# Kernel tuning notes

Measured on AMD Instinct MI355X. Metric: run time of the kernel, lower is better.

Reference implementation:

```python
import jax, jax.numpy as jnp
import numpy as np

H = 2048      # hidden
QL = 768      # q lora rank
KVL = 512     # kv lora rank
DR = 64       # rope dim
DN = 128      # nope head dim
NH = 16       # attention heads
NIH = 8       # indexer heads
IDX = 128     # indexer key dim
BS = 16       # batch
BLK = 128     # cache block size
BPS = 32      # blocks per sequence
NB = BS * BPS # total cache blocks
MAXKV = BPS * BLK  # 4096 kv slots per seq
TOPK = 1024   # sparse attention budget


def rmsnorm(v, g, eps=1e-6):
    return v * jax.lax.rsqrt(jnp.mean(v * v, -1, keepdims=True) + eps) * g


def layernorm(v, g, b, eps=1e-6):
    c = v - jnp.mean(v, -1, keepdims=True)
    return c * jax.lax.rsqrt(jnp.mean(c * c, -1, keepdims=True) + eps) * g + b


def rope(v, sin, cos):
    h = v.shape[-1] // 2
    rot = jnp.concatenate([-v[..., h:], v[..., :h]], -1)
    return v * cos + rot * sin


def setup_inputs() -> dict:
    key = jax.random.key(0)
    ks = jax.random.split(key, 16)
    s = 0.02  # weight init scale
    ang = jax.random.uniform(ks[5], (BS, 1, DR)) * 6.2831853
    return dict(
        x=jax.random.normal(ks[0], (BS, 1, H)),
        w_dq=jax.random.normal(ks[1], (H, QL)) * s,
        w_uq_qr=jax.random.normal(ks[2], (QL, NH * (DN + DR))) * s,
        w_uk=jax.random.normal(ks[3], (NH, DN, KVL)) * s,
        w_dkv_kr=jax.random.normal(ks[4], (H, KVL + DR)) * s,
        gamma_cq=jnp.ones((QL,)),
        gamma_ckv=jnp.ones((KVL,)),
        sin=jnp.sin(ang),
        cos=jnp.cos(ang),
        cache_index=jnp.arange(BS, dtype=jnp.int32) * MAXKV,
        kv_cache=jax.random.normal(ks[6], (NB, BLK, KVL)),
        kr_cache=jax.random.normal(ks[7], (NB, BLK, DR)),
        block_table=jnp.arange(BS * BPS, dtype=jnp.int32).reshape(BS, BPS),
        act_seqs=jnp.full((BS,), MAXKV, dtype=jnp.int32),
        w_idx_qb=jax.random.normal(ks[8], (QL, NIH * IDX)) * s,
        w_idx_k=jax.random.normal(ks[9], (H, IDX)) * s,
        w_idx_proj=jax.random.normal(ks[10], (QL, NIH)) * s,
        in_gamma_k=jnp.ones((IDX,)),
        in_beta_k=jnp.zeros((IDX,)),
        index_k_cache=jax.random.normal(ks[11], (NB, BLK, IDX)),
    )


def reference(x, w_dq, w_uq_qr, w_uk, w_dkv_kr, gamma_cq, gamma_ckv, sin, cos,
              cache_index, kv_cache, kr_cache, block_table, act_seqs,
              w_idx_qb, w_idx_k, w_idx_proj, in_gamma_k, in_beta_k, index_k_cache):
    bs = x.shape[0]
    xq = x[:, 0]                      # [bs, H] (decode, q_len=1)
    s0, c0 = sin[:, 0], cos[:, 0]     # [bs, DR]

    # --- low-rank Q path ---
    cq = rmsnorm(xq @ w_dq, gamma_cq)                           # [bs, QL]
    q = (cq @ w_uq_qr).reshape(bs, NH, DN + DR)
    q_nope, q_pe = q[..., :DN], q[..., DN:]
    q_pe = rope(q_pe, s0[:, None, :], c0[:, None, :])           # [bs, NH, DR]

    # --- latent KV path + cache write ---
    ckv_kr = xq @ w_dkv_kr
    ckv = rmsnorm(ckv_kr[:, :KVL], gamma_ckv)                   # [bs, KVL]
    kr = rope(ckv_kr[:, KVL:], s0, c0)                          # [bs, DR]
    kv_flat = kv_cache.reshape(NB * BLK, KVL).at[cache_index].set(ckv)
    kr_flat = kr_cache.reshape(NB * BLK, DR).at[cache_index].set(kr)

    # --- lightning indexer ---
    ki = layernorm(xq @ w_idx_k, in_gamma_k, in_beta_k)         # [bs, IDX]
    ik_flat = index_k_cache.reshape(NB * BLK, IDX).at[cache_index].set(ki)
    qi = (cq @ w_idx_qb).reshape(bs, NIH, IDX)
    head_w = cq @ w_idx_proj                                    # [bs, NIH]

    # paged gather: flat slot ids per sequence position
    pos = (block_table * BLK)[:, :, None] + jnp.arange(BLK, dtype=block_table.dtype)
    pos = pos.reshape(bs, MAXKV)                                # [bs, MAXKV]
    ki_all = ik_flat[pos]                                       # [bs, MAXKV, IDX]

    isc = jax.nn.relu(jnp.einsum('bhd,bnd->bhn', qi, ki_all))
    isc = jnp.einsum('bh,bhn->bn', head_w, isc) / jnp.sqrt(jnp.float32(IDX))
    mask = jnp.arange(MAXKV)[None, :] < act_seqs[:, None]
    isc = jnp.where(mask, isc, -1e9)
    top_s, top_i = jax.lax.top_k(isc, TOPK)                     # [bs, TOPK]

    sel = jnp.take_along_axis(pos, top_i, axis=1)               # [bs, TOPK]
    ckv_sel = kv_flat[sel]                                      # [bs, TOPK, KVL]
    kr_sel = kr_flat[sel]                                       # [bs, TOPK, DR]

    # --- absorbed MLA attention over selected tokens ---
    q_lat = jnp.einsum('bhd,hdc->bhc', q_nope, w_uk)            # [bs, NH, KVL]
    scale = 1.0 / np.sqrt(DN + DR)
    att = (jnp.einsum('bhc,bnc->bhn', q_lat, ckv_sel)
           + jnp.einsum('bhr,bnr->bhn', q_pe, kr_sel)) * scale
    att = jnp.where((top_s > -1e8)[:, None, :], att, -1e9)
    p = jax.nn.softmax(att, axis=-1)                            # [bs, NH, TOPK]
    o_lat = jnp.einsum('bhn,bnc->bhc', p, ckv_sel)              # [bs, NH, KVL]
    o = jnp.einsum('bhc,hdc->bhd', o_lat, w_uk)                 # [bs, NH, DN]
    return o.reshape(bs, 1, NH * DN)
```

## Files before the change

kernel.cpp:

```cpp
#include <hip/hip_runtime.h>

typedef unsigned int u32;

#define BS    16
#define HDIM  2048
#define QL    768
#define KVL   512
#define DR    64
#define DN    128
#define NH    16
#define NIH   8
#define IDXD  128
#define BLK   128
#define BPS   32
#define MAXKV 4096
#define TOPK  1024
#define NCH   32

__global__ void k_dproj(const float* __restrict__ x, const float* __restrict__ w_dq,
                        const float* __restrict__ w_dkv, const float* __restrict__ w_ik,
                        float* __restrict__ dpart){
  int tile = blockIdx.x, ks = blockIdx.y, t = threadIdx.x;
  __shared__ float xs[16*128];
  __shared__ float sred[8*32*17];
  int k0 = ks*128;
  for (int idx=t; idx<16*128; idx+=256){
    int bb=idx>>7, kk=idx&127;
    xs[idx] = x[bb*HDIM + k0 + kk];
  }
  const float* wp; int ld, c0, gbase;
  if (tile < 24){ wp=w_dq;  ld=768; c0=tile*32;      gbase=0; }
  else if (tile < 42){ wp=w_dkv; ld=576; c0=(tile-24)*32; gbase=768; }
  else { wp=w_ik;  ld=128; c0=(tile-42)*32; gbase=1344; }
  int cl = t&31, kg = t>>5;
  int col = c0 + cl;
  __syncthreads();
  float acc[16];
  #pragma unroll
  for (int bb=0;bb<16;bb++) acc[bb]=0.f;
  const float* wb = wp + (size_t)(k0 + kg*16)*ld + col;
  #pragma unroll 4
  for (int kk=0; kk<16; kk++){
    float wv = wb[(size_t)kk*ld];
    int kx = kg*16+kk;
    #pragma unroll
    for (int bb=0; bb<16; bb++) acc[bb] += xs[bb*128+kx]*wv;
  }
  #pragma unroll
  for (int bb=0;bb<16;bb++) sred[(kg*32+cl)*17+bb] = acc[bb];
  __syncthreads();
  for (int r=0; r<2; r++){
    int o = r*256 + t;
    int bb = o>>5, cl2 = o&31;
    float s=0.f;
    #pragma unroll
    for (int kg2=0; kg2<8; kg2++) s += sred[(kg2*32+cl2)*17+bb];
    dpart[((size_t)ks*16 + bb)*1472 + gbase + c0 + cl2] = s;
  }
}

__global__ void k_dfin(const float* __restrict__ dpart, const float* __restrict__ g_cq,
                       const float* __restrict__ g_ckv, const float* __restrict__ sinp,
                       const float* __restrict__ cosp, const float* __restrict__ g_ik,
                       const float* __restrict__ b_ik, const int* __restrict__ cidx,
                       float* __restrict__ cq, float* __restrict__ kvc,
                       float* __restrict__ krc, float* __restrict__ ikc){
  int b = blockIdx.x, t = threadIdx.x;
  __shared__ float val[1472];
  __shared__ float red[256];
  for (int c=t; c<1472; c+=256){
    float s = 0.f;
    for (int ks2=0; ks2<16; ks2++) s += dpart[((size_t)ks2*16+b)*1472 + c];
    val[c] = s;
  }
  __syncthreads();
  float c0v = val[t], c1v = val[t+256], c2v = val[t+512];
  red[t] = c0v*c0v + c1v*c1v + c2v*c2v;
  __syncthreads();
  for (int s=128;s>0;s>>=1){ if(t<s) red[t]+=red[t+s]; __syncthreads(); }
  float scq = 1.0f/sqrtf(red[0]/(float)QL + 1e-6f);
  __syncthreads();
  float v0 = val[768+t], v1 = val[1024+t];
  red[t] = v0*v0 + v1*v1;
  __syncthreads();
  for (int s=128;s>0;s>>=1){ if(t<s) red[t]+=red[t+s]; __syncthreads(); }
  float sckv = 1.0f/sqrtf(red[0]/(float)KVL + 1e-6f);
  __syncthreads();
  red[t] = (t<128)? val[1344+t] : 0.f;
  __syncthreads();
  for (int s=128;s>0;s>>=1){ if(t<s) red[t]+=red[t+s]; __syncthreads(); }
  float mean = red[0]/(float)IDXD;
  __syncthreads();
  float cc = (t<128)? (val[1344+t]-mean) : 0.f;
  red[t] = cc*cc;
  __syncthreads();
  for (int s=128;s>0;s>>=1){ if(t<s) red[t]+=red[t+s]; __syncthreads(); }
  float var = red[0]/(float)IDXD;
  int ci = cidx[b];
  cq[b*QL+t]     = c0v*scq*g_cq[t];
  cq[b*QL+t+256] = c1v*scq*g_cq[t+256];
  cq[b*QL+t+512] = c2v*scq*g_cq[t+512];
  kvc[(size_t)ci*KVL + t]     = v0*sckv*g_ckv[t];
  kvc[(size_t)ci*KVL + t+256] = v1*sckv*g_ckv[t+256];
  if (t<DR){
    float v = val[1280+t];
    float rot = (t<32)? -val[1280+t+32] : val[1280+t-32];
    krc[(size_t)ci*DR + t] = v*cosp[b*DR+t] + rot*sinp[b*DR+t];
  }
  if (t<IDXD){
    ikc[(size_t)ci*IDXD + t] = cc/sqrtf(var+1e-6f)*g_ik[t] + b_ik[t];
  }
}

__global__ void k_qall(const float* __restrict__ cq, const float* __restrict__ w_uq,
                       const float* __restrict__ w_qb, const float* __restrict__ w_pj,
                       float* __restrict__ qpart){
  int tile = blockIdx.x, ks = blockIdx.y, t = threadIdx.x;
  __shared__ float xs[16*192];
  __shared__ float sred[8*32*17];
  int k0 = ks*192;
  for (int idx=t; idx<16*192; idx+=256){
    int bb = idx/192, kk = idx - bb*192;
    xs[idx] = cq[bb*QL + k0 + kk];
  }
  const float* wp; int ld, c0, gbase, kind;
  if (tile < 96){ wp=w_uq; ld=3072; c0=tile*32; gbase=0; kind=0; }
  else if (tile < 128){ wp=w_qb; ld=1024; c0=(tile-96)*32; gbase=3072; kind=0; }
  else { wp=w_pj; ld=8; c0=0; gbase=4096; kind=1; }
  int cl = t&31, kg = t>>5;
  int col = c0 + cl;
  bool act = !(kind==1 && cl>=8);
  __syncthreads();
  float acc[16];
  #pragma unroll
  for (int bb=0;bb<16;bb++) acc[bb]=0.f;
  const float* wb = wp + (size_t)(k0 + kg*24)*ld + col;
  if (act){
    #pragma unroll 4
    for (int kk=0; kk<24; kk++){
      float wv = wb[(size_t)kk*ld];
      int kx = kg*24+kk;
      #pragma unroll
      for (int bb=0; bb<16; bb++) acc[bb] += xs[bb*192+kx]*wv;
    }
  }
  #pragma unroll
  for (int bb=0;bb<16;bb++) sred[(kg*32+cl)*17+bb] = acc[bb];
  __syncthreads();
  for (int r=0; r<2; r++){
    int o = r*256 + t;
    int bb = o>>5, cl2 = o&31;
    float s=0.f;
    #pragma unroll
    for (int kg2=0; kg2<8; kg2++) s += sred[(kg2*32+cl2)*17+bb];
    qpart[((size_t)ks*16 + bb)*4128 + gbase + c0 + cl2] = s;
  }
}

__global__ void k_qfin(const float* __restrict__ qpart, const float* __restrict__ sinp,
                       const float* __restrict__ cosp, float* __restrict__ qn,
                       float* __restrict__ qp, float* __restrict__ qi,
                       float* __restrict__ hw){
  int b=blockIdx.x, t=threadIdx.x;
  __shared__ float val[4104];
  for (int c=t; c<4104; c+=256){
    float s=0.f;
    for (int ks=0; ks<4; ks++) s += qpart[((size_t)ks*16+b)*4128 + c];
    val[c]=s;
  }
  __syncthreads();
  for (int c=t; c<4104; c+=256){
    if (c<3072){
      int h=c/192, j=c-h*192;
      if (j<128) qn[(b*NH+h)*DN+j] = val[c];
      else {
        int d=j-128;
        float v=val[c];
        float rot = (d<32)? -val[h*192+160+d] : val[h*192+96+d];
        qp[(b*NH+h)*DR+d] = v*cosp[b*DR+d] + rot*sinp[b*DR+d];
      }
    } else if (c<4096){
      qi[b*1024 + c-3072] = val[c];
    } else {
      hw[b*NIH + c-4096] = val[c];
    }
  }
}

__global__ void k_qlat(const float* __restrict__ qn, const float* __restrict__ wuk,
                       float* __restrict__ ql){
  int h=blockIdx.x, ct=blockIdx.y, t=threadIdx.x;
  __shared__ float qs[16*128];
  __shared__ float sred[4*64*17];
  for (int idx=t; idx<2048; idx+=256)
    qs[idx] = qn[((idx>>7)*NH+h)*DN + (idx&127)];
  int cl=t&63, kg=t>>6;
  int col=ct*64+cl;
  __syncthreads();
  float acc[16];
  #pragma unroll
  for (int bb=0;bb<16;bb++) acc[bb]=0.f;
  const float* wb = wuk + ((size_t)h*DN + kg*32)*KVL + col;
  #pragma unroll 4
  for (int kk=0;kk<32;kk++){
    float wv = wb[(size_t)kk*KVL];
    int kx = kg*32+kk;
    #pragma unroll
    for (int bb=0;bb<16;bb++) acc[bb]+=qs[bb*128+kx]*wv;
  }
  #pragma unroll
  for (int bb=0;bb<16;bb++) sred[(kg*64+cl)*17+bb]=acc[bb];
  __syncthreads();
  for (int r=0;r<4;r++){
    int o=r*256+t;
    int bb=o>>6, cl2=o&63;
    float s=0.f;
    #pragma unroll
    for (int kg2=0;kg2<4;kg2++) s+=sred[(kg2*64+cl2)*17+bb];
    ql[((size_t)bb*NH+h)*KVL + ct*64+cl2] = s;
  }
}

__global__ void k_isc(const float* __restrict__ qi, const float* __restrict__ hw,
                      const float* __restrict__ ikc, const int* __restrict__ btab,
                      const int* __restrict__ aseq, float* __restrict__ isc){
  int b=blockIdx.x, jb=blockIdx.y, t=threadIdx.x;
  __shared__ float K[64*129];
  __shared__ float qs[NIH*130];
  __shared__ float hs[NIH];
  __shared__ float red[64*4];
  int blk = btab[b*BPS+jb];
  for (int idx=t; idx<NIH*IDXD; idx+=256){ int h2=idx>>7, d=idx&127; qs[h2*130+d]=qi[b*1024+idx]; }
  if (t<NIH) hs[t]=hw[b*NIH+t];
  const float4* k4 = (const float4*)(ikc + (size_t)blk*BLK*IDXD);
  int as = aseq[b];
  int r = t>>2, hp = t&3;
  for (int half=0; half<2; half++){
    __syncthreads();
    for (int it=0; it<8; it++){
      int idx = it*256 + t;
      int rr = idx>>5, c4 = idx&31;
      float4 v = k4[(half*64+rr)*32 + c4];
      float* dst = &K[rr*129 + c4*4];
      dst[0]=v.x; dst[1]=v.y; dst[2]=v.z; dst[3]=v.w;
    }
    __syncthreads();
    float s0=0.f, s1=0.f;
    const float* Kr = &K[r*129];
    const float* q0 = &qs[hp*130];
    const float* q1 = &qs[(hp+4)*130];
    for (int d=0; d<IDXD; d++){
      float kv = Kr[d];
      s0 += q0[d]*kv; s1 += q1[d]*kv;
    }
    red[r*4+hp] = hs[hp]*fmaxf(s0,0.f) + hs[hp+4]*fmaxf(s1,0.f);
    __syncthreads();
    if (t<64){
      float sc = (red[t*4]+red[t*4+1]+red[t*4+2]+red[t*4+3]) * 0.08838834764831845f;
      int n = jb*BLK + half*64 + t;
      if (n >= as) sc = -1e9f;
      isc[b*MAXKV + n] = sc;
    }
  }
}

__global__ void k_topk(const float* __restrict__ isc, const int* __restrict__ btab,
                       int* __restrict__ selp, float* __restrict__ sels){
  int b=blockIdx.x, t=threadIdx.x;
  int lane = t&63, wv = t>>6;
  __shared__ u32 su[MAXKV];
  __shared__ u32 hist[256];
  __shared__ u32 cum[256];
  __shared__ u32 wtot[4];
  __shared__ u32 sh_b;
  for (int k2=0;k2<16;k2++){
    int i=k2*256+t;
    u32 bits=__float_as_uint(isc[b*MAXKV+i]);
    su[i] = (bits & 0x80000000u) ? ~bits : (bits | 0x80000000u);
  }
  u32 prefix=0u, need=1024u;
  for (int shift=24; shift>=0; shift-=8){
    hist[t]=0u;
    __syncthreads();
    u32 hm = (shift==24)? 0u : (0xFFFFFFFFu << (shift+8));
    for (int j=0;j<16;j++){
      u32 u = su[t*16+j];
      if ((u & hm) == prefix) atomicAdd(&hist[(u>>shift)&255u], 1u);
    }
    __syncthreads();
    u32 v = hist[wv*64+lane];
    for (int off=1; off<64; off<<=1){
      u32 tmp = __shfl_down(v, off);
      if (lane + off < 64) v += tmp;
    }
    if (lane==0) wtot[wv]=v;
    __syncthreads();
    u32 add=0u;
    for (int w2=wv+1; w2<4; w2++) add += wtot[w2];
    v += add;
    cum[wv*64+lane] = v;
    __syncthreads();
    int bin = wv*64+lane;
    u32 nxt = (bin<255)? cum[bin+1] : 0u;
    if (v>=need && nxt<need) sh_b = (u32)bin;
    __syncthreads();
    u32 B = sh_b;
    u32 aboveB = (B<255u)? cum[B+1] : 0u;
    need -= aboveB;
    prefix |= (B<<shift);
    __syncthreads();
  }
  u32 T = prefix;
  u32 cG=0u,cE=0u;
  for (int j=0;j<16;j++){ u32 u=su[t*16+j]; cG += (u>T)?1u:0u; cE += (u==T)?1u:0u; }
  u32 packed = (cG<<16) | cE;
  u32 v = packed;
  for (int off=1; off<64; off<<=1){
    u32 tmp = __shfl_up(v, off);
    if (lane >= off) v += tmp;
  }
  if (lane==63) wtot[wv]=v;
  __syncthreads();
  u32 add=0u;
  for (int w2=0; w2<wv; w2++) add += wtot[w2];
  u32 excl = v + add - packed;
  u32 total = wtot[0]+wtot[1]+wtot[2]+wtot[3];
  u32 mGT = total>>16;
  u32 keepEq = 1024u - mGT;
  u32 gG = excl>>16, gE = excl&0xFFFFu;
  for (int j=0;j<16;j++){
    int i=t*16+j; u32 u=su[i];
    int slot=-1;
    if (u>T) slot=(int)(gG++);
    else if (u==T){ u32 r2=gE++; if (r2<keepEq) slot=(int)(mGT+r2); }
    if (slot>=0){
      int pos = btab[b*BPS + (i>>7)]*BLK + (i&127);
      selp[b*TOPK+slot]=pos;
      sels[b*TOPK+slot]=isc[b*MAXKV+i];
    }
  }
}

__global__ void k_fgat(const float* __restrict__ qlat, const float* __restrict__ qpe,
                       const float* __restrict__ kvc, const float* __restrict__ krc,
                       const int* __restrict__ selp, const float* __restrict__ sels,
                       float* __restrict__ opart, float* __restrict__ mch,
                       float* __restrict__ lch){
  int b=blockIdx.x, ch=blockIdx.y, t=threadIdx.x;
  __shared__ float K[16*580];
  __shared__ float sS[16*17];
  __shared__ float sM[16], sL[16], sA[16];
  __shared__ int   sp[32];
  __shared__ float sv[32];
  if (t<32){ sp[t]=selp[b*TOPK+ch*32+t]; sv[t]=sels[b*TOPK+ch*32+t]; }
  if (t<16){ sM[t]=-1e30f; sL[t]=0.f; }
  int h = t>>4, i = t&15;
  int hg = t>>6, c4 = t&63;
  const float4* qc  = (const float4*)(qlat + ((size_t)b*NH+h)*KVL);
  const float4* qp4 = (const float4*)(qpe  + ((size_t)b*NH+h)*DR);
  const float4* kv4 = (const float4*)kvc;
  const float4* kr4 = (const float4*)krc;
  float4 acc[8];
  #pragma unroll
  for (int j=0;j<8;j++){ acc[j].x=0.f; acc[j].y=0.f; acc[j].z=0.f; acc[j].w=0.f; }
  const float scale = 0.07216878364870323f;
  for (int st=0; st<2; st++){
    __syncthreads();
    for (int idx=t; idx<16*128; idx+=256){
      int r=idx>>7, cc=idx&127;
      ((float4*)&K[r*580])[cc] = kv4[(size_t)sp[st*16+r]*128 + cc];
    }
    for (int idx=t; idx<16*16; idx+=256){
      int r=idx>>4, cc=idx&15;
      ((float4*)&K[r*580])[128+cc] = kr4[(size_t)sp[st*16+r]*16 + cc];
    }
    __syncthreads();
    const float4* Kr4 = (const float4*)&K[i*580];
    float s=0.f;
    for (int v=0; v<128; v++){
      float4 q = qc[v]; float4 kk = Kr4[v];
      s += kk.x*q.x + kk.y*q.y + kk.z*q.z + kk.w*q.w;
    }
    for (int v=0; v<16; v++){
      float4 q = qp4[v]; float4 kk = Kr4[128+v];
      s += kk.x*q.x + kk.y*q.y + kk.z*q.z + kk.w*q.w;
    }
    float val = (sv[st*16+i] > -1e8f)? s*scale : -1e9f;
    float mx = val;
    for (int mm=1; mm<16; mm<<=1) mx = fmaxf(mx, __shfl_xor(mx, mm, 16));
    float mold = sM[h];
    float mnew = fmaxf(mold, mx);
    float p = expf(val - mnew);
    float psum = p;
    for (int mm=1; mm<16; mm<<=1) psum += __shfl_xor(psum, mm, 16);
    sS[h*17+i] = p;
    if (i==0){
      float al = expf(mold - mnew);
      sA[h] = al;
      sM[h] = mnew;
      sL[h] = sL[h]*al + psum;
    }
    __syncthreads();
    #pragma unroll
    for (int j=0;j<4;j++){
      int hh = hg*4+j;
      float al = sA[hh];
      float4 a0=acc[j*2], a1=acc[j*2+1];
      a0.x*=al; a0.y*=al; a0.z*=al; a0.w*=al;
      a1.x*=al; a1.y*=al; a1.z*=al; a1.w*=al;
      for (int rr=0; rr<16; rr++){
        float pv = sS[hh*17+rr];
        const float4* KrR = (const float4*)&K[rr*580];
        float4 k0 = KrR[c4], k1 = KrR[64+c4];
        a0.x += pv*k0.x; a0.y += pv*k0.y; a0.z += pv*k0.z; a0.w += pv*k0.w;
        a1.x += pv*k1.x; a1.y += pv*k1.y; a1.z += pv*k1.z; a1.w += pv*k1.w;
      }
      acc[j*2]=a0; acc[j*2+1]=a1;
    }
  }
  __syncthreads();
  #pragma unroll
  for (int j=0;j<4;j++){
    int hh = hg*4+j;
    float4* dst = (float4*)(opart + (((size_t)(b*NCH+ch))*NH + hh)*KVL);
    dst[c4]    = acc[j*2];
    dst[64+c4] = acc[j*2+1];
  }
  if (t<16){
    mch[(b*NCH+ch)*16 + t] = sM[t];
    lch[(b*NCH+ch)*16 + t] = sL[t];
  }
}

__global__ void k_comb(const float* __restrict__ opart, const float* __restrict__ mch,
                       const float* __restrict__ lch, const float* __restrict__ wuk,
                       float* __restrict__ out){
  int b=blockIdx.x, h=blockIdx.y, t=threadIdx.x;
  __shared__ float sOl[KVL];
  __shared__ float sCoef[NCH];
  __shared__ float sInvL;
  if (t<NCH){
    float mv = mch[(b*NCH+t)*16+h];
    float lv = lch[(b*NCH+t)*16+h];
    float M = mv;
    for (int off=1; off<NCH; off<<=1) M = fmaxf(M, __shfl_xor(M, off, NCH));
    float coef = expf(mv - M);
    float Lp = lv*coef;
    for (int off=1; off<NCH; off<<=1) Lp += __shfl_xor(Lp, off, NCH);
    sCoef[t] = coef;
    if (t==0) sInvL = 1.0f/Lp;
  }
  __syncthreads();
  for (int c=t; c<KVL; c+=128){
    float s=0.f;
    for (int ch=0; ch<NCH; ch++)
      s += opart[(((size_t)(b*NCH+ch))*NH + h)*KVL + c] * sCoef[ch];
    sOl[c] = s*sInvL;
  }
  __syncthreads();
  const float4* w4 = (const float4*)(wuk + ((size_t)(h*DN)+t)*KVL);
  const float4* o4 = (const float4*)sOl;
  float a=0.f;
  for (int v=0; v<128; v++){
    float4 w = w4[v]; float4 o = o4[v];
    a += w.x*o.x + w.y*o.y + w.z*o.z + w.w*o.w;
  }
  out[b*(NH*DN) + h*DN + t] = a;
}

extern "C" void kernel_launch(void* const* d_in, const int* in_sizes, int n_in,
                              void* d_out, int out_size, void* d_ws, size_t ws_size,
                              hipStream_t stream){
  const float* x        =(const float*)d_in[0];
  const float* w_dq     =(const float*)d_in[1];
  const float* w_uq_qr  =(const float*)d_in[2];
  const float* w_uk     =(const float*)d_in[3];
  const float* w_dkv_kr =(const float*)d_in[4];
  const float* g_cq     =(const float*)d_in[5];
  const float* g_ckv    =(const float*)d_in[6];
  const float* sinp     =(const float*)d_in[7];
  const float* cosp     =(const float*)d_in[8];
  const int*   cidx     =(const int*)d_in[9];
  float*       kvc      =(float*)d_in[10];
  float*       krc      =(float*)d_in[11];
  const int*   btab     =(const int*)d_in[12];
  const int*   aseq     =(const int*)d_in[13];
  const float* w_idx_qb =(const float*)d_in[14];
  const float* w_idx_k  =(const float*)d_in[15];
  const float* w_idx_pj =(const float*)d_in[16];
  const float* g_ik     =(const float*)d_in[17];
  const float* b_ik     =(const float*)d_in[18];
  float*       ikc      =(float*)d_in[19];

  float* ws    = (float*)d_ws;
  float* cq    = ws;
  float* qnope = ws + 12288;
  float* qpe   = ws + 45056;
  float* qlat  = ws + 61440;
  float* qi    = ws + 192512;
  float* hw    = ws + 208896;
  float* isc   = ws + 209024;
  int*   selp  = (int*)(ws + 274560);
  float* sels  = ws + 290944;
  float* dpart = ws + 307328;
  float* qpart = ws + 684160;
  float* mch   = ws + 948352;
  float* lch   = ws + 956544;
  float* opart = ws + 964736;

  k_dproj<<<dim3(46,16),  dim3(256),0,stream>>>(x,w_dq,w_dkv_kr,w_idx_k,dpart);
  k_dfin <<<dim3(BS),     dim3(256),0,stream>>>(dpart,g_cq,g_ckv,sinp,cosp,g_ik,b_ik,cidx,cq,kvc,krc,ikc);
  k_qall <<<dim3(129,4),  dim3(256),0,stream>>>(cq,w_uq_qr,w_idx_qb,w_idx_pj,qpart);
  k_qfin <<<dim3(BS),     dim3(256),0,stream>>>(qpart,sinp,cosp,qnope,qpe,qi,hw);
  k_qlat <<<dim3(16,8),   dim3(256),0,stream>>>(qnope,w_uk,qlat);
  k_isc  <<<dim3(BS,BPS), dim3(256),0,stream>>>(qi,hw,ikc,btab,aseq,isc);
  k_topk <<<dim3(BS),     dim3(256),0,stream>>>(isc,btab,selp,sels);
  k_fgat <<<dim3(BS,NCH), dim3(256),0,stream>>>(qlat,qpe,kvc,krc,selp,sels,opart,mch,lch);
  k_comb <<<dim3(BS,NH),  dim3(128),0,stream>>>(opart,mch,lch,w_uk,(float*)d_out);
}
```

Measured before the change: 398.2 us.

## Restructure sparse attention gather with register prefetch and wider per-block chunks

The fused gather-attention kernel now handles 64 selected tokens per block with 512 threads, halving the chunk count that the combine kernel merges. Both 32-row stages are loaded into registers up front, and the second stage is written to shared memory only after the first has been computed, so its global latency overlaps the first stage's math. Each head gets 32 lanes that keep the online-softmax state and accumulators in registers, which removes the shared-memory max/sum bookkeeping and several barriers. In exchange it uses about 148 KB of LDS per block and many more registers, which limits occupancy to one block per CU.

```diff
diff --git a/kernel.cpp b/kernel.cpp
--- a/kernel.cpp
+++ b/kernel.cpp
@@ -15,7 +15,7 @@
 #define BPS   32
 #define MAXKV 4096
 #define TOPK  1024
-#define NCH   32
+#define NCH   16
 
 __global__ void k_dproj(const float* __restrict__ x, const float* __restrict__ w_dq,
                         const float* __restrict__ w_dkv, const float* __restrict__ w_ik,
@@ -341,94 +341,114 @@
   }
 }
 
-__global__ void k_fgat(const float* __restrict__ qlat, const float* __restrict__ qpe,
-                       const float* __restrict__ kvc, const float* __restrict__ krc,
-                       const int* __restrict__ selp, const float* __restrict__ sels,
-                       float* __restrict__ opart, float* __restrict__ mch,
-                       float* __restrict__ lch){
+#define FGAT_STAGE(ROWOFF)                                                    \
+  {                                                                           \
+    const float4* Kr = (const float4*)&K[(ROWOFF+ir)*580];                    \
+    float s=0.f;                                                              \
+    _Pragma("unroll 8")                                                       \
+    for (int v=0;v<128;v++){ float4 q=qc[v], k=Kr[v];                         \
+      s += q.x*k.x+q.y*k.y+q.z*k.z+q.w*k.w; }                                 \
+    _Pragma("unroll")                                                         \
+    for (int v=0;v<16;v++){ float4 q=qp4[v], k=Kr[128+v];                     \
+      s += q.x*k.x+q.y*k.y+q.z*k.z+q.w*k.w; }                                 \
+    float val = (sv[ROWOFF+ir] > -1e8f)? s*scale : -1e9f;                     \
+    float mx = val;                                                           \
+    _Pragma("unroll")                                                         \
+    for (int mm=1;mm<32;mm<<=1) mx = fmaxf(mx, __shfl_xor(mx, mm, 32));       \
+    float mnew = fmaxf(m_run, mx);                                            \
+    float p = expf(val - mnew);                                               \
+    float ps = p;                                                             \
+    _Pragma("unroll")                                                         \
+    for (int mm=1;mm<32;mm<<=1) ps += __shfl_xor(ps, mm, 32);                 \
+    float al = expf(m_run - mnew);                                            \
+    l_run = l_run*al + ps; m_run = mnew;                                      \
+    sS[hs*33+ir] = p;                                                         \
+    acc0.x*=al; acc0.y*=al; acc0.z*=al; acc0.w*=al;                           \
+    acc1.x*=al; acc1.y*=al; acc1.z*=al; acc1.w*=al;                           \
+    acc2.x*=al; acc2.y*=al; acc2.z*=al; acc2.w*=al;                           \
+    acc3.x*=al; acc3.y*=al; acc3.z*=al; acc3.w*=al;                           \
+    _Pragma("unroll 4")                                                       \
+    for (int r=0;r<32;r++){                                                   \
+      float pv = sS[hs*33+r];                                                 \
+      const float4* KrR = (const float4*)&K[(ROWOFF+r)*580];                  \
+      float4 k0=KrR[ir], k1=KrR[32+ir], k2=KrR[64+ir], k3=KrR[96+ir];         \
+      acc0.x+=pv*k0.x; acc0.y+=pv*k0.y; acc0.z+=pv*k0.z; acc0.w+=pv*k0.w;     \
+      acc1.x+=pv*k1.x; acc1.y+=pv*k1.y; acc1.z+=pv*k1.z; acc1.w+=pv*k1.w;     \
+      acc2.x+=pv*k2.x; acc2.y+=pv*k2.y; acc2.z+=pv*k2.z; acc2.w+=pv*k2.w;     \
+      acc3.x+=pv*k3.x; acc3.y+=pv*k3.y; acc3.z+=pv*k3.z; acc3.w+=pv*k3.w;     \
+    }                                                                         \
+  }
+
+__global__ __launch_bounds__(512, 2)
+void k_fgat(const float* __restrict__ qlat, const float* __restrict__ qpe,
+            const float* __restrict__ kvc, const float* __restrict__ krc,
+            const int* __restrict__ selp, const float* __restrict__ sels,
+            float* __restrict__ opart, float* __restrict__ mch,
+            float* __restrict__ lch){
   int b=blockIdx.x, ch=blockIdx.y, t=threadIdx.x;
-  __shared__ float K[16*580];
-  __shared__ float sS[16*17];
-  __shared__ float sM[16], sL[16], sA[16];
-  __shared__ int   sp[32];
-  __shared__ float sv[32];
-  if (t<32){ sp[t]=selp[b*TOPK+ch*32+t]; sv[t]=sels[b*TOPK+ch*32+t]; }
-  if (t<16){ sM[t]=-1e30f; sL[t]=0.f; }
-  int h = t>>4, i = t&15;
-  int hg = t>>6, c4 = t&63;
-  const float4* qc  = (const float4*)(qlat + ((size_t)b*NH+h)*KVL);
-  const float4* qp4 = (const float4*)(qpe  + ((size_t)b*NH+h)*DR);
+  __shared__ float K[2*32*580];
+  __shared__ float sS[16*33];
+  __shared__ int   sp[64];
+  __shared__ float sv[64];
+  if (t<64){ sp[t]=selp[b*TOPK+ch*64+t]; sv[t]=sels[b*TOPK+ch*64+t]; }
+  __syncthreads();
+
   const float4* kv4 = (const float4*)kvc;
   const float4* kr4 = (const float4*)krc;
-  float4 acc[8];
-  #pragma unroll
-  for (int j=0;j<8;j++){ acc[j].x=0.f; acc[j].y=0.f; acc[j].z=0.f; acc[j].w=0.f; }
+  float4 rA[9], rB[9];
+  #pragma unroll
+  for (int j=0;j<9;j++){
+    int idx=j*512+t, r=idx/144, c=idx-r*144;
+    const float4* src = (c<128)? (kv4 + (size_t)sp[r]*128 + c)
+                               : (kr4 + (size_t)sp[r]*16 + (c-128));
+    rA[j] = *src;
+  }
+  #pragma unroll
+  for (int j=0;j<9;j++){
+    int idx=j*512+t, r=idx/144, c=idx-r*144;
+    const float4* src = (c<128)? (kv4 + (size_t)sp[32+r]*128 + c)
+                               : (kr4 + (size_t)sp[32+r]*16 + (c-128));
+    rB[j] = *src;
+  }
+  #pragma unroll
+  for (int j=0;j<9;j++){
+    int idx=j*512+t, r=idx/144, c=idx-r*144;
+    ((float4*)&K[r*580])[c] = rA[j];
+  }
+  asm volatile("s_waitcnt lgkmcnt(0)" ::: "memory");
+  __builtin_amdgcn_s_barrier();
+
+  int hs = t>>5;
+  int ir = t&31;
+  const float4* qc  = (const float4*)(qlat + ((size_t)b*NH+hs)*KVL);
+  const float4* qp4 = (const float4*)(qpe  + ((size_t)b*NH+hs)*DR);
   const float scale = 0.07216878364870323f;
-  for (int st=0; st<2; st++){
-    __syncthreads();
-    for (int idx=t; idx<16*128; idx+=256){
-      int r=idx>>7, cc=idx&127;
-      ((float4*)&K[r*580])[cc] = kv4[(size_t)sp[st*16+r]*128 + cc];
-    }
-    for (int idx=t; idx<16*16; idx+=256){
-      int r=idx>>4, cc=idx&15;
-      ((float4*)&K[r*580])[128+cc] = kr4[(size_t)sp[st*16+r]*16 + cc];
-    }
-    __syncthreads();
-    const float4* Kr4 = (const float4*)&K[i*580];
-    float s=0.f;
-    for (int v=0; v<128; v++){
-      float4 q = qc[v]; float4 kk = Kr4[v];
-      s += kk.x*q.x + kk.y*q.y + kk.z*q.z + kk.w*q.w;
-    }
-    for (int v=0; v<16; v++){
-      float4 q = qp4[v]; float4 kk = Kr4[128+v];
-      s += kk.x*q.x + kk.y*q.y + kk.z*q.z + kk.w*q.w;
-    }
-    float val = (sv[st*16+i] > -1e8f)? s*scale : -1e9f;
-    float mx = val;
-    for (int mm=1; mm<16; mm<<=1) mx = fmaxf(mx, __shfl_xor(mx, mm, 16));
-    float mold = sM[h];
-    float mnew = fmaxf(mold, mx);
-    float p = expf(val - mnew);
-    float psum = p;
-    for (int mm=1; mm<16; mm<<=1) psum += __shfl_xor(psum, mm, 16);
-    sS[h*17+i] = p;
-    if (i==0){
-      float al = expf(mold - mnew);
-      sA[h] = al;
-      sM[h] = mnew;
-      sL[h] = sL[h]*al + psum;
-    }
-    __syncthreads();
-    #pragma unroll
-    for (int j=0;j<4;j++){
-      int hh = hg*4+j;
-      float al = sA[hh];
-      float4 a0=acc[j*2], a1=acc[j*2+1];
-      a0.x*=al; a0.y*=al; a0.z*=al; a0.w*=al;
-      a1.x*=al; a1.y*=al; a1.z*=al; a1.w*=al;
-      for (int rr=0; rr<16; rr++){
-        float pv = sS[hh*17+rr];
-        const float4* KrR = (const float4*)&K[rr*580];
-        float4 k0 = KrR[c4], k1 = KrR[64+c4];
-        a0.x += pv*k0.x; a0.y += pv*k0.y; a0.z += pv*k0.z; a0.w += pv*k0.w;
-        a1.x += pv*k1.x; a1.y += pv*k1.y; a1.z += pv*k1.z; a1.w += pv*k1.w;
-      }
-      acc[j*2]=a0; acc[j*2+1]=a1;
-    }
-  }
-  __syncthreads();
-  #pragma unroll
-  for (int j=0;j<4;j++){
-    int hh = hg*4+j;
-    float4* dst = (float4*)(opart + (((size_t)(b*NCH+ch))*NH + hh)*KVL);
-    dst[c4]    = acc[j*2];
-    dst[64+c4] = acc[j*2+1];
-  }
-  if (t<16){
-    mch[(b*NCH+ch)*16 + t] = sM[t];
-    lch[(b*NCH+ch)*16 + t] = sL[t];
+  float m_run=-1e30f, l_run=0.f;
+  float4 acc0,acc1,acc2,acc3;
+  acc0.x=acc0.y=acc0.z=acc0.w=0.f;
+  acc1.x=acc1.y=acc1.z=acc1.w=0.f;
+  acc2.x=acc2.y=acc2.z=acc2.w=0.f;
+  acc3.x=acc3.y=acc3.z=acc3.w=0.f;
+
+  FGAT_STAGE(0)
+
+  #pragma unroll
+  for (int j=0;j<9;j++){
+    int idx=j*512+t, r=idx/144, c=idx-r*144;
+    ((float4*)&K[(32+r)*580])[c] = rB[j];
+  }
+  __syncthreads();
+
+  FGAT_STAGE(32)
+
+  float4* dst = (float4*)(opart + (((size_t)(b*NCH+ch))*NH + hs)*KVL);
+  dst[ir]    = acc0;
+  dst[32+ir] = acc1;
+  dst[64+ir] = acc2;
+  dst[96+ir] = acc3;
+  if (ir==0){
+    mch[(b*NCH+ch)*16 + hs] = m_run;
+    lch[(b*NCH+ch)*16 + hs] = l_run;
   }
 }
 
@@ -515,6 +535,6 @@
   k_qlat <<<dim3(16,8),   dim3(256),0,stream>>>(qnope,w_uk,qlat);
   k_isc  <<<dim3(BS,BPS), dim3(256),0,stream>>>(qi,hw,ikc,btab,aseq,isc);
   k_topk <<<dim3(BS),     dim3(256),0,stream>>>(isc,btab,selp,sels);
-  k_fgat <<<dim3(BS,NCH), dim3(256),0,stream>>>(qlat,qpe,kvc,krc,selp,sels,opart,mch,lch);
+  k_fgat <<<dim3(BS,NCH), dim3(512),0,stream>>>(qlat,qpe,kvc,krc,selp,sels,opart,mch,lch);
   k_comb <<<dim3(BS,NH),  dim3(128),0,stream>>>(opart,mch,lch,w_uk,(float*)d_out);
 }
```

Result: faster. 362.1 us (-9.1%).

## Split finalize kernels across more blocks and restructure sparse gather-attention chunk

Applied to the files above, without the earlier changes.

The dproj finalize kernel is split into three blocks per batch (q-norm, kv-norm plus rope, indexer layernorm), and the q finalize kernel into 17 blocks per batch, so these serial per-batch reductions run on more CUs in parallel. The gather-attention kernel now loads all 32 selected rows at once through registers into a larger shared tile, keeps q in registers, splits each score dot product across 16 lanes, and does a single softmax per chunk with no online rescaling. It also uses shuffles to broadcast probabilities and swaps the grid order. The larger shared tile and register arrays raise per-block resource use, which could limit occupancy.

```diff
diff --git a/kernel.cpp b/kernel.cpp
--- a/kernel.cpp
+++ b/kernel.cpp
@@ -65,50 +65,65 @@
                        const float* __restrict__ b_ik, const int* __restrict__ cidx,
                        float* __restrict__ cq, float* __restrict__ kvc,
                        float* __restrict__ krc, float* __restrict__ ikc){
-  int b = blockIdx.x, t = threadIdx.x;
-  __shared__ float val[1472];
+  int b = blockIdx.x, sec = blockIdx.y, t = threadIdx.x;
+  __shared__ float val[768];
   __shared__ float red[256];
-  for (int c=t; c<1472; c+=256){
-    float s = 0.f;
-    for (int ks2=0; ks2<16; ks2++) s += dpart[((size_t)ks2*16+b)*1472 + c];
-    val[c] = s;
-  }
-  __syncthreads();
-  float c0v = val[t], c1v = val[t+256], c2v = val[t+512];
-  red[t] = c0v*c0v + c1v*c1v + c2v*c2v;
-  __syncthreads();
-  for (int s=128;s>0;s>>=1){ if(t<s) red[t]+=red[t+s]; __syncthreads(); }
-  float scq = 1.0f/sqrtf(red[0]/(float)QL + 1e-6f);
-  __syncthreads();
-  float v0 = val[768+t], v1 = val[1024+t];
-  red[t] = v0*v0 + v1*v1;
-  __syncthreads();
-  for (int s=128;s>0;s>>=1){ if(t<s) red[t]+=red[t+s]; __syncthreads(); }
-  float sckv = 1.0f/sqrtf(red[0]/(float)KVL + 1e-6f);
-  __syncthreads();
-  red[t] = (t<128)? val[1344+t] : 0.f;
-  __syncthreads();
-  for (int s=128;s>0;s>>=1){ if(t<s) red[t]+=red[t+s]; __syncthreads(); }
-  float mean = red[0]/(float)IDXD;
-  __syncthreads();
-  float cc = (t<128)? (val[1344+t]-mean) : 0.f;
-  red[t] = cc*cc;
-  __syncthreads();
-  for (int s=128;s>0;s>>=1){ if(t<s) red[t]+=red[t+s]; __syncthreads(); }
-  float var = red[0]/(float)IDXD;
-  int ci = cidx[b];
-  cq[b*QL+t]     = c0v*scq*g_cq[t];
-  cq[b*QL+t+256] = c1v*scq*g_cq[t+256];
-  cq[b*QL+t+512] = c2v*scq*g_cq[t+512];
-  kvc[(size_t)ci*KVL + t]     = v0*sckv*g_ckv[t];
-  kvc[(size_t)ci*KVL + t+256] = v1*sckv*g_ckv[t+256];
-  if (t<DR){
-    float v = val[1280+t];
-    float rot = (t<32)? -val[1280+t+32] : val[1280+t-32];
-    krc[(size_t)ci*DR + t] = v*cosp[b*DR+t] + rot*sinp[b*DR+t];
-  }
-  if (t<IDXD){
-    ikc[(size_t)ci*IDXD + t] = cc/sqrtf(var+1e-6f)*g_ik[t] + b_ik[t];
+  if (sec==0){
+    for (int c=t; c<768; c+=256){
+      float s = 0.f;
+      for (int ks2=0; ks2<16; ks2++) s += dpart[((size_t)ks2*16+b)*1472 + c];
+      val[c] = s;
+    }
+    __syncthreads();
+    float c0v = val[t], c1v = val[t+256], c2v = val[t+512];
+    red[t] = c0v*c0v + c1v*c1v + c2v*c2v;
+    __syncthreads();
+    for (int s=128;s>0;s>>=1){ if(t<s) red[t]+=red[t+s]; __syncthreads(); }
+    float scq = 1.0f/sqrtf(red[0]/(float)QL + 1e-6f);
+    cq[b*QL+t]     = c0v*scq*g_cq[t];
+    cq[b*QL+t+256] = c1v*scq*g_cq[t+256];
+    cq[b*QL+t+512] = c2v*scq*g_cq[t+512];
+  } else if (sec==1){
+    for (int c=t; c<576; c+=256){
+      float s = 0.f;
+      for (int ks2=0; ks2<16; ks2++) s += dpart[((size_t)ks2*16+b)*1472 + 768 + c];
+      val[c] = s;
+    }
+    __syncthreads();
+    float v0 = val[t], v1 = val[t+256];
+    red[t] = v0*v0 + v1*v1;
+    __syncthreads();
+    for (int s=128;s>0;s>>=1){ if(t<s) red[t]+=red[t+s]; __syncthreads(); }
+    float sckv = 1.0f/sqrtf(red[0]/(float)KVL + 1e-6f);
+    int ci = cidx[b];
+    kvc[(size_t)ci*KVL + t]     = v0*sckv*g_ckv[t];
+    kvc[(size_t)ci*KVL + t+256] = v1*sckv*g_ckv[t+256];
+    if (t<DR){
+      float v = val[512+t];
+      float rot = (t<32)? -val[512+t+32] : val[512+t-32];
+      krc[(size_t)ci*DR + t] = v*cosp[b*DR+t] + rot*sinp[b*DR+t];
+    }
+  } else {
+    for (int c=t; c<128; c+=256){
+      float s = 0.f;
+      for (int ks2=0; ks2<16; ks2++) s += dpart[((size_t)ks2*16+b)*1472 + 1344 + c];
+      val[c] = s;
+    }
+    __syncthreads();
+    red[t] = (t<128)? val[t] : 0.f;
+    __syncthreads();
+    for (int s=128;s>0;s>>=1){ if(t<s) red[t]+=red[t+s]; __syncthreads(); }
+    float mean = red[0]/(float)IDXD;
+    __syncthreads();
+    float cc = (t<128)? (val[t]-mean) : 0.f;
+    red[t] = cc*cc;
+    __syncthreads();
+    for (int s=128;s>0;s>>=1){ if(t<s) red[t]+=red[t+s]; __syncthreads(); }
+    float var = red[0]/(float)IDXD;
+    int ci = cidx[b];
+    if (t<IDXD){
+      ikc[(size_t)ci*IDXD + t] = cc/sqrtf(var+1e-6f)*g_ik[t] + b_ik[t];
+    }
   }
 }
 
@@ -161,28 +176,34 @@
                        const float* __restrict__ cosp, float* __restrict__ qn,
                        float* __restrict__ qp, float* __restrict__ qi,
                        float* __restrict__ hw){
-  int b=blockIdx.x, t=threadIdx.x;
-  __shared__ float val[4104];
-  for (int c=t; c<4104; c+=256){
-    float s=0.f;
-    for (int ks=0; ks<4; ks++) s += qpart[((size_t)ks*16+b)*4128 + c];
-    val[c]=s;
-  }
-  __syncthreads();
-  for (int c=t; c<4104; c+=256){
-    if (c<3072){
-      int h=c/192, j=c-h*192;
-      if (j<128) qn[(b*NH+h)*DN+j] = val[c];
+  int b=blockIdx.x, part=blockIdx.y, t=threadIdx.x;
+  if (part<16){
+    __shared__ float val[192];
+    int h=part;
+    if (t<192){
+      int c = h*192 + t;
+      float s=0.f;
+      for (int ks=0; ks<4; ks++) s += qpart[((size_t)ks*16+b)*4128 + c];
+      val[t]=s;
+    }
+    __syncthreads();
+    if (t<192){
+      int j=t;
+      if (j<128) qn[(b*NH+h)*DN+j] = val[j];
       else {
         int d=j-128;
-        float v=val[c];
-        float rot = (d<32)? -val[h*192+160+d] : val[h*192+96+d];
+        float v=val[j];
+        float rot = (d<32)? -val[160+d] : val[96+d];
         qp[(b*NH+h)*DR+d] = v*cosp[b*DR+d] + rot*sinp[b*DR+d];
       }
-    } else if (c<4096){
-      qi[b*1024 + c-3072] = val[c];
-    } else {
-      hw[b*NIH + c-4096] = val[c];
+    }
+  } else {
+    for (int idx=t; idx<1032; idx+=256){
+      int c = 3072+idx;
+      float s=0.f;
+      for (int ks=0; ks<4; ks++) s += qpart[((size_t)ks*16+b)*4128 + c];
+      if (idx<1024) qi[b*1024 + idx] = s;
+      else hw[b*NIH + idx-1024] = s;
     }
   }
 }
@@ -341,94 +362,101 @@
   }
 }
 
-__global__ void k_fgat(const float* __restrict__ qlat, const float* __restrict__ qpe,
-                       const float* __restrict__ kvc, const float* __restrict__ krc,
-                       const int* __restrict__ selp, const float* __restrict__ sels,
-                       float* __restrict__ opart, float* __restrict__ mch,
-                       float* __restrict__ lch){
-  int b=blockIdx.x, ch=blockIdx.y, t=threadIdx.x;
-  __shared__ float K[16*580];
-  __shared__ float sS[16*17];
-  __shared__ float sM[16], sL[16], sA[16];
-  __shared__ int   sp[32];
-  __shared__ float sv[32];
-  if (t<32){ sp[t]=selp[b*TOPK+ch*32+t]; sv[t]=sels[b*TOPK+ch*32+t]; }
-  if (t<16){ sM[t]=-1e30f; sL[t]=0.f; }
-  int h = t>>4, i = t&15;
-  int hg = t>>6, c4 = t&63;
-  const float4* qc  = (const float4*)(qlat + ((size_t)b*NH+h)*KVL);
-  const float4* qp4 = (const float4*)(qpe  + ((size_t)b*NH+h)*DR);
+__global__ __launch_bounds__(256, 2)
+void k_fgat(const float* __restrict__ qlat, const float* __restrict__ qpe,
+            const float* __restrict__ kvc, const float* __restrict__ krc,
+            const int* __restrict__ selp, const float* __restrict__ sels,
+            float* __restrict__ opart, float* __restrict__ mch,
+            float* __restrict__ lch){
+  int ch=blockIdx.x, b=blockIdx.y, t=threadIdx.x;
+  __shared__ float K[32*580];
+  int lane31 = t&31;
+  int sp_l   = selp[b*TOPK + ch*32 + lane31];
+  float sv_l = sels[b*TOPK + ch*32 + lane31];
   const float4* kv4 = (const float4*)kvc;
   const float4* kr4 = (const float4*)krc;
-  float4 acc[8];
-  #pragma unroll
-  for (int j=0;j<8;j++){ acc[j].x=0.f; acc[j].y=0.f; acc[j].z=0.f; acc[j].w=0.f; }
+  float4 rA[18];
+  #pragma unroll
+  for (int j=0;j<18;j++){
+    int idx=j*256+t, r=idx/144, c=idx-r*144;
+    int row = __shfl(sp_l, r, 64);
+    rA[j] = (c<128)? kv4[(size_t)row*128 + c] : kr4[(size_t)row*16 + (c-128)];
+  }
+  int h = t>>4, kc = t&15;
+  const float4* ql4 = (const float4*)(qlat + ((size_t)b*NH+h)*KVL);
+  const float4* qp4 = (const float4*)(qpe  + ((size_t)b*NH+h)*DR);
+  float4 qreg[9];
+  #pragma unroll
+  for (int j=0;j<9;j++){
+    int g = kc*9 + j;
+    qreg[j] = (g<128)? ql4[g] : qp4[g-128];
+  }
+  #pragma unroll
+  for (int j=0;j<18;j++){
+    int idx=j*256+t, r=idx/144, c=idx-r*144;
+    ((float4*)&K[r*580])[c] = rA[j];
+  }
+  __syncthreads();
   const float scale = 0.07216878364870323f;
-  for (int st=0; st<2; st++){
-    __syncthreads();
-    for (int idx=t; idx<16*128; idx+=256){
-      int r=idx>>7, cc=idx&127;
-      ((float4*)&K[r*580])[cc] = kv4[(size_t)sp[st*16+r]*128 + cc];
-    }
-    for (int idx=t; idx<16*16; idx+=256){
-      int r=idx>>4, cc=idx&15;
-      ((float4*)&K[r*580])[128+cc] = kr4[(size_t)sp[st*16+r]*16 + cc];
-    }
-    __syncthreads();
-    const float4* Kr4 = (const float4*)&K[i*580];
+  float pa=0.f, pb=0.f;
+  for (int r=0;r<32;r++){
+    const float4* Kc = (const float4*)&K[r*580 + kc*36];
     float s=0.f;
-    for (int v=0; v<128; v++){
-      float4 q = qc[v]; float4 kk = Kr4[v];
-      s += kk.x*q.x + kk.y*q.y + kk.z*q.z + kk.w*q.w;
-    }
-    for (int v=0; v<16; v++){
-      float4 q = qp4[v]; float4 kk = Kr4[128+v];
-      s += kk.x*q.x + kk.y*q.y + kk.z*q.z + kk.w*q.w;
-    }
-    float val = (sv[st*16+i] > -1e8f)? s*scale : -1e9f;
-    float mx = val;
-    for (int mm=1; mm<16; mm<<=1) mx = fmaxf(mx, __shfl_xor(mx, mm, 16));
-    float mold = sM[h];
-    float mnew = fmaxf(mold, mx);
-    float p = expf(val - mnew);
-    float psum = p;
-    for (int mm=1; mm<16; mm<<=1) psum += __shfl_xor(psum, mm, 16);
-    sS[h*17+i] = p;
-    if (i==0){
-      float al = expf(mold - mnew);
-      sA[h] = al;
-      sM[h] = mnew;
-      sL[h] = sL[h]*al + psum;
-    }
-    __syncthreads();
-    #pragma unroll
-    for (int j=0;j<4;j++){
-      int hh = hg*4+j;
-      float al = sA[hh];
-      float4 a0=acc[j*2], a1=acc[j*2+1];
-      a0.x*=al; a0.y*=al; a0.z*=al; a0.w*=al;
-      a1.x*=al; a1.y*=al; a1.z*=al; a1.w*=al;
-      for (int rr=0; rr<16; rr++){
-        float pv = sS[hh*17+rr];
-        const float4* KrR = (const float4*)&K[rr*580];
-        float4 k0 = KrR[c4], k1 = KrR[64+c4];
-        a0.x += pv*k0.x; a0.y += pv*k0.y; a0.z += pv*k0.z; a0.w += pv*k0.w;
-        a1.x += pv*k1.x; a1.y += pv*k1.y; a1.z += pv*k1.z; a1.w += pv*k1.w;
-      }
-      acc[j*2]=a0; acc[j*2+1]=a1;
-    }
-  }
-  __syncthreads();
-  #pragma unroll
-  for (int j=0;j<4;j++){
-    int hh = hg*4+j;
+    #pragma unroll
+    for (int j=0;j<9;j++){
+      float4 kv=Kc[j], q=qreg[j];
+      s += kv.x*q.x + kv.y*q.y + kv.z*q.z + kv.w*q.w;
+    }
+    #pragma unroll
+    for (int mm=1;mm<16;mm<<=1) s += __shfl_xor(s, mm, 16);
+    float svr = __shfl(sv_l, r, 64);
+    float val = (svr > -1e8f)? s*scale : -1e9f;
+    if (r<16) pa = (kc==r)?      val : pa;
+    else      pb = (kc==(r-16))? val : pb;
+  }
+  float m2 = fmaxf(pa, pb);
+  #pragma unroll
+  for (int mm=1;mm<16;mm<<=1) m2 = fmaxf(m2, __shfl_xor(m2, mm, 16));
+  pa = expf(pa - m2); pb = expf(pb - m2);
+  float l2 = pa + pb;
+  #pragma unroll
+  for (int mm=1;mm<16;mm<<=1) l2 += __shfl_xor(l2, mm, 16);
+  int l6 = t&63;
+  float4 a0[4], a1[4];
+  #pragma unroll
+  for (int hq=0;hq<4;hq++){
+    a0[hq].x=a0[hq].y=a0[hq].z=a0[hq].w=0.f;
+    a1[hq].x=a1[hq].y=a1[hq].z=a1[hq].w=0.f;
+  }
+  for (int r=0;r<32;r++){
+    const float4* Vr = (const float4*)&K[r*580];
+    float4 v0 = Vr[l6], v1 = Vr[64+l6];
+    float ps = (r<16)? pa : pb;
+    int srcl = (r&15);
+    float p0 = __shfl(ps, srcl,      64);
+    float p1 = __shfl(ps, 16+srcl,   64);
+    float p2 = __shfl(ps, 32+srcl,   64);
+    float p3 = __shfl(ps, 48+srcl,   64);
+    a0[0].x+=p0*v0.x; a0[0].y+=p0*v0.y; a0[0].z+=p0*v0.z; a0[0].w+=p0*v0.w;
+    a1[0].x+=p0*v1.x; a1[0].y+=p0*v1.y; a1[0].z+=p0*v1.z; a1[0].w+=p0*v1.w;
+    a0[1].x+=p1*v0.x; a0[1].y+=p1*v0.y; a0[1].z+=p1*v0.z; a0[1].w+=p1*v0.w;
+    a1[1].x+=p1*v1.x; a1[1].y+=p1*v1.y; a1[1].z+=p1*v1.z; a1[1].w+=p1*v1.w;
+    a0[2].x+=p2*v0.x; a0[2].y+=p2*v0.y; a0[2].z+=p2*v0.z; a0[2].w+=p2*v0.w;
+    a1[2].x+=p2*v1.x; a1[2].y+=p2*v1.y; a1[2].z+=p2*v1.z; a1[2].w+=p2*v1.w;
+    a0[3].x+=p3*v0.x; a0[3].y+=p3*v0.y; a0[3].z+=p3*v0.z; a0[3].w+=p3*v0.w;
+    a1[3].x+=p3*v1.x; a1[3].y+=p3*v1.y; a1[3].z+=p3*v1.z; a1[3].w+=p3*v1.w;
+  }
+  int wv = t>>6;
+  #pragma unroll
+  for (int hq=0;hq<4;hq++){
+    int hh = wv*4 + hq;
     float4* dst = (float4*)(opart + (((size_t)(b*NCH+ch))*NH + hh)*KVL);
-    dst[c4]    = acc[j*2];
-    dst[64+c4] = acc[j*2+1];
-  }
-  if (t<16){
-    mch[(b*NCH+ch)*16 + t] = sM[t];
-    lch[(b*NCH+ch)*16 + t] = sL[t];
+    dst[l6]    = a0[hq];
+    dst[64+l6] = a1[hq];
+  }
+  if (kc==0){
+    mch[(b*NCH+ch)*16 + h] = m2;
+    lch[(b*NCH+ch)*16 + h] = l2;
   }
 }
 
@@ -509,12 +537,12 @@
   float* opart = ws + 964736;
 
   k_dproj<<<dim3(46,16),  dim3(256),0,stream>>>(x,w_dq,w_dkv_kr,w_idx_k,dpart);
-  k_dfin <<<dim3(BS),     dim3(256),0,stream>>>(dpart,g_cq,g_ckv,sinp,cosp,g_ik,b_ik,cidx,cq,kvc,krc,ikc);
+  k_dfin <<<dim3(BS,3),   dim3(256),0,stream>>>(dpart,g_cq,g_ckv,sinp,cosp,g_ik,b_ik,cidx,cq,kvc,krc,ikc);
   k_qall <<<dim3(129,4),  dim3(256),0,stream>>>(cq,w_uq_qr,w_idx_qb,w_idx_pj,qpart);
-  k_qfin <<<dim3(BS),     dim3(256),0,stream>>>(qpart,sinp,cosp,qnope,qpe,qi,hw);
+  k_qfin <<<dim3(BS,17),  dim3(256),0,stream>>>(qpart,sinp,cosp,qnope,qpe,qi,hw);
   k_qlat <<<dim3(16,8),   dim3(256),0,stream>>>(qnope,w_uk,qlat);
   k_isc  <<<dim3(BS,BPS), dim3(256),0,stream>>>(qi,hw,ikc,btab,aseq,isc);
   k_topk <<<dim3(BS),     dim3(256),0,stream>>>(isc,btab,selp,sels);
-  k_fgat <<<dim3(BS,NCH), dim3(256),0,stream>>>(qlat,qpe,kvc,krc,selp,sels,opart,mch,lch);
+  k_fgat <<<dim3(NCH,BS), dim3(256),0,stream>>>(qlat,qpe,kvc,krc,selp,sels,opart,mch,lch);
   k_comb <<<dim3(BS,NH),  dim3(128),0,stream>>>(opart,mch,lch,w_uk,(float*)d_out);
 }
```

After: 344.7 us. -13.4%, faster.
